# Optimization experiments

Hardware: AMD Instinct MI355X
Metric: run time of the kernel (lower is better)

## Reference

```python
import jax, jax.numpy as jnp
import numpy as np


def setup_inputs() -> dict:
    key = jax.random.key(0)
    k1, k2, k3 = jax.random.split(key, 3)
    N, Ci, H, W = 16, 64, 224, 224
    Co, K = 128, 3
    x = jax.random.normal(k1, (N, Ci, H, W), dtype=jnp.float32)
    # Kaiming-like scale for conv weight
    conv_weight = jax.random.normal(k2, (Co, Ci, K, K), dtype=jnp.float32) * (1.0 / np.sqrt(Ci * K * K))
    conv_bias = jax.random.normal(k3, (Co,), dtype=jnp.float32) * 0.01
    return {"x": x, "conv_weight": conv_weight, "conv_bias": conv_bias}


def reference(x, conv_weight, conv_bias):
    # conv2d, stride=1, padding=0 (VALID), NCHW / OIHW
    y = jax.lax.conv_general_dilated(
        x, conv_weight,
        window_strides=(1, 1),
        padding="VALID",
        dimension_numbers=("NCHW", "OIHW", "NCHW"),
    ) + conv_bias[None, :, None, None]  # [N, Co, OH, OW]
    # min over output channels (keepdim), then double tanh
    m = jnp.min(y, axis=1, keepdims=True)  # [N, 1, OH, OW]
    return jnp.tanh(jnp.tanh(m))
```

## Files before the change

### kernel.cpp

```cpp
#include <hip/hip_runtime.h>
#include <hip/hip_bf16.h>
#include <math.h>

#define NN   16
#define CI   64
#define HH   224
#define WW   224
#define CO   128
#define OHH  222
#define OWW  222

#define WS_NEED (36*4*64*16)

typedef short  short8  __attribute__((ext_vector_type(8)));
typedef float  f32x16  __attribute__((ext_vector_type(16)));
typedef float  f32x4   __attribute__((ext_vector_type(4)));

__device__ static inline unsigned f2bf_pk(float a, float b) {
  __hip_bfloat162 h = __float22bfloat162_rn(make_float2(a, b));
  return *reinterpret_cast<unsigned*>(&h);
}

__global__ __launch_bounds__(256) void prep_w_kernel(const float* __restrict__ wt,
                                                     unsigned char* __restrict__ ws) {
  int t    = blockIdx.x * 256 + threadIdx.x;
  int lane = t & 63;
  int f    = t >> 6;
  int s    = f >> 2;
  int ct   = f & 3;
  int tap  = s >> 2;
  int cic  = s & 3;
  int kh   = tap / 3, kw = tap % 3;
  int co   = ct * 32 + (lane & 31);
  int k0   = cic * 16 + (lane >> 5) * 8;
  unsigned pk[4];
#pragma unroll
  for (int j = 0; j < 4; ++j) {
    int ci0 = k0 + 2 * j;
    float a = wt[(size_t)co * 576 + (ci0    ) * 9 + kh * 3 + kw];
    float b = wt[(size_t)co * 576 + (ci0 + 1) * 9 + kh * 3 + kw];
    pk[j] = f2bf_pk(a, b);
  }
  ((uint4*)ws)[t] = make_uint4(pk[0], pk[1], pk[2], pk[3]);
}

__global__ __launch_bounds__(256, 2) void conv_min_kernel(
    const float* __restrict__ x, const float* __restrict__ bias,
    const unsigned char* __restrict__ ws, float* __restrict__ out) {
  __shared__ __align__(16) unsigned char smem[6 * 72 * 128];

  int bid  = blockIdx.x;
  int owt  = bid & 3;
  int rest = bid >> 2;
  int oht  = rest % 56;
  int n    = rest / 56;
  int ow0  = (owt < 3) ? owt * 64 : 158;
  int oh0  = oht * 4;

  int tid   = threadIdx.x;
  int wv    = tid >> 6;
  int lane  = tid & 63;
  int mg    = wv >> 1;
  int ng    = wv & 1;
  int mrow  = lane & 31;
  int khalf = lane >> 5;

  const short8* wf = (const short8*)ws;
  int bbase = ng * 128 + lane;
  short8 bb[3][2];
#pragma unroll
  for (int ct = 0; ct < 2; ++ct) bb[0][ct] = wf[0 * 256 + ct * 64 + bbase];
#pragma unroll
  for (int ct = 0; ct < 2; ++ct) bb[1][ct] = wf[1 * 256 + ct * 64 + bbase];

  {
    int colm = (tid & 31) * 2;
    int q    = (tid >> 5) & 7;
    int cole = 64 + (tid & 7);
    int ppe  = tid >> 3;
    const float* xb = x + (size_t)n * 64 * 50176;
#pragma unroll 1
    for (int r = 0; r < 6; ++r) {
      int rg = oh0 + r; if (rg > 223) rg = 223;
      const float* xr = xb + (size_t)rg * 224;
#pragma unroll
      for (int p = 0; p < 4; ++p) {
        int pp = p * 8 + q;
        int ci = pp * 2;
        const float* s0 = xr + (size_t)ci * 50176 + ow0 + colm;
        float2 a2 = *(const float2*)s0;
        float2 b2 = *(const float2*)(s0 + 50176);
        unsigned u0 = f2bf_pk(a2.x, b2.x);
        unsigned u1 = f2bf_pk(a2.y, b2.y);
        int cc = pp >> 2, jw = (pp & 3) * 4;
        *(unsigned*)(smem + (r * 72 + colm    ) * 128 + (((cc + colm    ) & 7) << 4) + jw) = u0;
        *(unsigned*)(smem + (r * 72 + colm + 1) * 128 + (((cc + colm + 1) & 7) << 4) + jw) = u1;
      }
      {
        int colg = ow0 + cole; if (colg > 223) colg = 223;
        const float* s0 = xr + (size_t)(ppe * 2) * 50176 + colg;
        float a = s0[0], b = s0[50176];
        *(unsigned*)(smem + (r * 72 + cole) * 128 + ((((ppe >> 2) + cole) & 7) << 4) + (ppe & 3) * 4) =
            f2bf_pk(a, b);
      }
    }
  }

  f32x16 acc[4][2];
#pragma unroll
  for (int ct = 0; ct < 2; ++ct) {
    float bv = bias[ng * 64 + ct * 32 + mrow];
#pragma unroll
    for (int mtl = 0; mtl < 4; ++mtl)
#pragma unroll
      for (int r = 0; r < 16; ++r) acc[mtl][ct][r] = bv;
  }

  unsigned uu = (mrow + khalf) & 7;
  const unsigned char* Pb = smem + mg * 18432 + mrow * 128;
  const unsigned char* P[8];
#pragma unroll
  for (int j = 0; j < 8; ++j) P[j] = Pb + ((uu + j) & 7) * 16;

  __syncthreads();

  short8 aa[2][4];
#pragma unroll
  for (int mtl = 0; mtl < 4; ++mtl) {
    const int ohl = mtl >> 1, owh = mtl & 1;
    aa[0][mtl] = *(const short8*)(P[0] + ((ohl * 72 + owh * 32) << 7));
  }

#pragma unroll
  for (int s = 0; s < 36; ++s) {
    if (s + 2 < 36) {
#pragma unroll
      for (int ct = 0; ct < 2; ++ct)
        bb[(s + 2) % 3][ct] = wf[(s + 2) * 256 + ct * 64 + bbase];
    }
    if (s + 1 < 36) {
      const int s1 = s + 1;
      const int kh1 = s1 / 12, kw1 = (s1 / 4) % 3, cic1 = s1 & 3;
      const int j1 = (2 * cic1 + kw1) & 7;
#pragma unroll
      for (int mtl = 0; mtl < 4; ++mtl) {
        const int ohl = mtl >> 1, owh = mtl & 1;
        aa[s1 & 1][mtl] =
            *(const short8*)(P[j1] + ((((ohl + kh1) * 72) + kw1 + owh * 32) << 7));
      }
    }
#pragma unroll
    for (int mtl = 0; mtl < 4; ++mtl)
#pragma unroll
      for (int ct = 0; ct < 2; ++ct)
        acc[mtl][ct] = __builtin_amdgcn_mfma_f32_32x32x16_bf16(
            aa[s & 1][mtl], bb[s % 3][ct], acc[mtl][ct], 0, 0, 0);
  }

  __syncthreads();
  float* epi = (float*)smem;
#pragma unroll
  for (int mtl = 0; mtl < 4; ++mtl) {
    const int ohl = mtl >> 1, owh = mtl & 1;
#pragma unroll
    for (int r = 0; r < 16; ++r) {
      float v = fminf(acc[mtl][0][r], acc[mtl][1][r]);
      v = fminf(v, __shfl_xor(v, 16, 64));
      if ((lane & 16) == 0) {
        int px = (mg * 2 + ohl) * 64 + owh * 32 + ((r & 3) + 8 * (r >> 2) + 4 * khalf);
        epi[px * 36 + ng * 16 + (lane & 15)] = v;
      }
    }
  }
  __syncthreads();
  {
    int px = tid;
    int rowsel = px >> 6;
    int oh = oh0 + rowsel;
    const f32x4* rowp = (const f32x4*)(epi + px * 36);
    f32x4 m4 = rowp[0];
#pragma unroll
    for (int k = 1; k < 8; ++k) {
      f32x4 t = rowp[k];
      m4[0] = fminf(m4[0], t[0]); m4[1] = fminf(m4[1], t[1]);
      m4[2] = fminf(m4[2], t[2]); m4[3] = fminf(m4[3], t[3]);
    }
    float v = fminf(fminf(m4[0], m4[1]), fminf(m4[2], m4[3]));
    v = tanhf(tanhf(v));
    if (oh < OHH)
      out[(size_t)n * (OHH * OWW) + (size_t)oh * OWW + ow0 + (px & 63)] = v;
  }
}

__global__ __launch_bounds__(128) void fallback_kernel(
    const float* __restrict__ x, const float* __restrict__ wt,
    const float* __restrict__ bias, float* __restrict__ out) {
  __shared__ float patch[64 * 30];
  __shared__ float red[128];
  int pb   = blockIdx.x;
  int owt  = pb % 28;
  int rest = pb / 28;
  int oh   = rest % OHH;
  int n    = rest / OHH;
  int ow0  = owt * 8;
  int tid  = threadIdx.x;
  for (int i = tid; i < 1920; i += 128) {
    int wl = i % 10;
    int rr = (i / 10) % 3;
    int ci = i / 30;
    int wg = ow0 + wl;
    float v = 0.f;
    if (wg < WW) v = x[((size_t)(n * 64 + ci) * HH + (oh + rr)) * WW + wg];
    patch[i] = v;
  }
  __syncthreads();
  int co = tid;
  float a[8];
#pragma unroll
  for (int p = 0; p < 8; ++p) a[p] = bias[co];
  for (int ci = 0; ci < 64; ++ci) {
#pragma unroll
    for (int rr = 0; rr < 3; ++rr)
#pragma unroll
      for (int kw = 0; kw < 3; ++kw) {
        float wvv = wt[(size_t)co * 576 + ci * 9 + rr * 3 + kw];
        const float* pp = &patch[ci * 30 + rr * 10 + kw];
#pragma unroll
        for (int p = 0; p < 8; ++p) a[p] += pp[p] * wvv;
      }
  }
  for (int p = 0; p < 8; ++p) {
    red[tid] = a[p];
    __syncthreads();
    for (int st = 64; st > 0; st >>= 1) {
      if (tid < st) red[tid] = fminf(red[tid], red[tid + st]);
      __syncthreads();
    }
    if (tid == 0 && (ow0 + p) < OWW)
      out[(size_t)n * (OHH * OWW) + (size_t)oh * OWW + ow0 + p] = tanhf(tanhf(red[0]));
    __syncthreads();
  }
}

extern "C" void kernel_launch(void* const* d_in, const int* in_sizes, int n_in,
                              void* d_out, int out_size, void* d_ws, size_t ws_size,
                              hipStream_t stream) {
  const float* x    = (const float*)d_in[0];
  const float* wt   = (const float*)d_in[1];
  const float* bias = (const float*)d_in[2];
  float* out        = (float*)d_out;

  if (ws_size >= WS_NEED) {
    unsigned char* ws = (unsigned char*)d_ws;
    prep_w_kernel<<<36, 256, 0, stream>>>(wt, ws);
    conv_min_kernel<<<NN * 56 * 4, 256, 0, stream>>>(x, bias, ws, out);
  } else {
    fallback_kernel<<<NN * OHH * 28, 128, 0, stream>>>(x, wt, bias, out);
  }
}
```

Measured before the change: 414.6 us.

## Shrink output tile width to 32 columns and raise occupancy to 4 blocks/CU

Each block now covers 4 rows by 32 output columns instead of 64, with half the accumulators and a smaller LDS input patch. Launch bounds ask for 4 blocks per SM, and the block index is permuted in groups of 8 to spread neighbouring tiles across XCDs. The aim is more resident waves to hide global-load and LDS latency and less wasted work on the last column tile. In exchange, halo and weight reloads per output pixel go up and the epilogue uses only half the threads.

```diff
diff --git a/kernel.cpp b/kernel.cpp
--- a/kernel.cpp
+++ b/kernel.cpp
@@ -44,17 +44,19 @@
   ((uint4*)ws)[t] = make_uint4(pk[0], pk[1], pk[2], pk[3]);
 }
 
-__global__ __launch_bounds__(256, 2) void conv_min_kernel(
+__global__ __launch_bounds__(256, 4) void conv_min_kernel(
     const float* __restrict__ x, const float* __restrict__ bias,
     const unsigned char* __restrict__ ws, float* __restrict__ out) {
-  __shared__ __align__(16) unsigned char smem[6 * 72 * 128];
-
-  int bid  = blockIdx.x;
-  int owt  = bid & 3;
-  int rest = bid >> 2;
+  __shared__ __align__(16) unsigned char smem[6 * 34 * 128];
+
+  int bid = blockIdx.x;
+  bid = (bid & 7) * (NN * 56 * 7 / 8) + (bid >> 3);
+
+  int owt  = bid % 7;
+  int rest = bid / 7;
   int oht  = rest % 56;
   int n    = rest / 56;
-  int ow0  = (owt < 3) ? owt * 64 : 158;
+  int ow0  = (owt < 6) ? owt * 32 : 190;
   int oh0  = oht * 4;
 
   int tid   = threadIdx.x;
@@ -74,18 +76,16 @@
   for (int ct = 0; ct < 2; ++ct) bb[1][ct] = wf[1 * 256 + ct * 64 + bbase];
 
   {
-    int colm = (tid & 31) * 2;
-    int q    = (tid >> 5) & 7;
-    int cole = 64 + (tid & 7);
-    int ppe  = tid >> 3;
+    int colm = (tid & 15) * 2;
+    int q    = tid >> 4;
     const float* xb = x + (size_t)n * 64 * 50176;
 #pragma unroll 1
     for (int r = 0; r < 6; ++r) {
       int rg = oh0 + r; if (rg > 223) rg = 223;
       const float* xr = xb + (size_t)rg * 224;
 #pragma unroll
-      for (int p = 0; p < 4; ++p) {
-        int pp = p * 8 + q;
+      for (int p = 0; p < 2; ++p) {
+        int pp = p * 16 + q;
         int ci = pp * 2;
         const float* s0 = xr + (size_t)ci * 50176 + ow0 + colm;
         float2 a2 = *(const float2*)s0;
@@ -93,43 +93,42 @@
         unsigned u0 = f2bf_pk(a2.x, b2.x);
         unsigned u1 = f2bf_pk(a2.y, b2.y);
         int cc = pp >> 2, jw = (pp & 3) * 4;
-        *(unsigned*)(smem + (r * 72 + colm    ) * 128 + (((cc + colm    ) & 7) << 4) + jw) = u0;
-        *(unsigned*)(smem + (r * 72 + colm + 1) * 128 + (((cc + colm + 1) & 7) << 4) + jw) = u1;
-      }
-      {
-        int colg = ow0 + cole; if (colg > 223) colg = 223;
-        const float* s0 = xr + (size_t)(ppe * 2) * 50176 + colg;
+        *(unsigned*)(smem + (r * 34 + colm    ) * 128 + (((cc + colm    ) & 7) << 4) + jw) = u0;
+        *(unsigned*)(smem + (r * 34 + colm + 1) * 128 + (((cc + colm + 1) & 7) << 4) + jw) = u1;
+      }
+      if (tid < 64) {
+        int cole = 32 + (tid & 1);
+        int ppe  = tid >> 1;
+        const float* s0 = xr + (size_t)(ppe * 2) * 50176 + ow0 + cole;
         float a = s0[0], b = s0[50176];
-        *(unsigned*)(smem + (r * 72 + cole) * 128 + ((((ppe >> 2) + cole) & 7) << 4) + (ppe & 3) * 4) =
+        *(unsigned*)(smem + (r * 34 + cole) * 128 + ((((ppe >> 2) + cole) & 7) << 4) + (ppe & 3) * 4) =
             f2bf_pk(a, b);
       }
     }
   }
 
-  f32x16 acc[4][2];
+  f32x16 acc[2][2];
 #pragma unroll
   for (int ct = 0; ct < 2; ++ct) {
     float bv = bias[ng * 64 + ct * 32 + mrow];
 #pragma unroll
-    for (int mtl = 0; mtl < 4; ++mtl)
-#pragma unroll
-      for (int r = 0; r < 16; ++r) acc[mtl][ct][r] = bv;
+    for (int ohl = 0; ohl < 2; ++ohl)
+#pragma unroll
+      for (int r = 0; r < 16; ++r) acc[ohl][ct][r] = bv;
   }
 
   unsigned uu = (mrow + khalf) & 7;
-  const unsigned char* Pb = smem + mg * 18432 + mrow * 128;
+  const unsigned char* Pb = smem + mg * (2 * 34 * 128) + mrow * 128;
   const unsigned char* P[8];
 #pragma unroll
   for (int j = 0; j < 8; ++j) P[j] = Pb + ((uu + j) & 7) * 16;
 
   __syncthreads();
 
-  short8 aa[2][4];
-#pragma unroll
-  for (int mtl = 0; mtl < 4; ++mtl) {
-    const int ohl = mtl >> 1, owh = mtl & 1;
-    aa[0][mtl] = *(const short8*)(P[0] + ((ohl * 72 + owh * 32) << 7));
-  }
+  short8 aa[2][2];
+#pragma unroll
+  for (int ohl = 0; ohl < 2; ++ohl)
+    aa[0][ohl] = *(const short8*)(P[0] + ((ohl * 34) << 7));
 
 #pragma unroll
   for (int s = 0; s < 36; ++s) {
@@ -143,40 +142,36 @@
       const int kh1 = s1 / 12, kw1 = (s1 / 4) % 3, cic1 = s1 & 3;
       const int j1 = (2 * cic1 + kw1) & 7;
 #pragma unroll
-      for (int mtl = 0; mtl < 4; ++mtl) {
-        const int ohl = mtl >> 1, owh = mtl & 1;
-        aa[s1 & 1][mtl] =
-            *(const short8*)(P[j1] + ((((ohl + kh1) * 72) + kw1 + owh * 32) << 7));
-      }
-    }
-#pragma unroll
-    for (int mtl = 0; mtl < 4; ++mtl)
+      for (int ohl = 0; ohl < 2; ++ohl)
+        aa[s1 & 1][ohl] =
+            *(const short8*)(P[j1] + ((((ohl + kh1) * 34) + kw1) << 7));
+    }
+#pragma unroll
+    for (int ohl = 0; ohl < 2; ++ohl)
 #pragma unroll
       for (int ct = 0; ct < 2; ++ct)
-        acc[mtl][ct] = __builtin_amdgcn_mfma_f32_32x32x16_bf16(
-            aa[s & 1][mtl], bb[s % 3][ct], acc[mtl][ct], 0, 0, 0);
+        acc[ohl][ct] = __builtin_amdgcn_mfma_f32_32x32x16_bf16(
+            aa[s & 1][ohl], bb[s % 3][ct], acc[ohl][ct], 0, 0, 0);
   }
 
   __syncthreads();
   float* epi = (float*)smem;
 #pragma unroll
-  for (int mtl = 0; mtl < 4; ++mtl) {
-    const int ohl = mtl >> 1, owh = mtl & 1;
+  for (int ohl = 0; ohl < 2; ++ohl) {
 #pragma unroll
     for (int r = 0; r < 16; ++r) {
-      float v = fminf(acc[mtl][0][r], acc[mtl][1][r]);
+      float v = fminf(acc[ohl][0][r], acc[ohl][1][r]);
       v = fminf(v, __shfl_xor(v, 16, 64));
       if ((lane & 16) == 0) {
-        int px = (mg * 2 + ohl) * 64 + owh * 32 + ((r & 3) + 8 * (r >> 2) + 4 * khalf);
+        int px = (mg * 2 + ohl) * 32 + ((r & 3) + 8 * (r >> 2) + 4 * khalf);
         epi[px * 36 + ng * 16 + (lane & 15)] = v;
       }
     }
   }
   __syncthreads();
-  {
+  if (tid < 128) {
     int px = tid;
-    int rowsel = px >> 6;
-    int oh = oh0 + rowsel;
+    int oh = oh0 + (px >> 5);
     const f32x4* rowp = (const f32x4*)(epi + px * 36);
     f32x4 m4 = rowp[0];
 #pragma unroll
@@ -188,7 +183,7 @@
     float v = fminf(fminf(m4[0], m4[1]), fminf(m4[2], m4[3]));
     v = tanhf(tanhf(v));
     if (oh < OHH)
-      out[(size_t)n * (OHH * OWW) + (size_t)oh * OWW + ow0 + (px & 63)] = v;
+      out[(size_t)n * (OHH * OWW) + (size_t)oh * OWW + ow0 + (px & 31)] = v;
   }
 }
 
@@ -253,7 +248,7 @@
   if (ws_size >= WS_NEED) {
     unsigned char* ws = (unsigned char*)d_ws;
     prep_w_kernel<<<36, 256, 0, stream>>>(wt, ws);
-    conv_min_kernel<<<NN * 56 * 4, 256, 0, stream>>>(x, bias, ws, out);
+    conv_min_kernel<<<NN * 56 * 7, 256, 0, stream>>>(x, bias, ws, out);
   } else {
     fallback_kernel<<<NN * OHH * 28, 128, 0, stream>>>(x, wt, bias, out);
   }
```

After: 428.5 us. 3.4% more time.
